# Kernel optimization log

Hardware: AMD Instinct MI355X
Metric: run time of the kernel (lower is better)

Reference implementation:

```python
import jax, jax.numpy as jnp
import numpy as np

B, N, M, C = 2, 8192, 8192, 3
SRC_W = 1.0  # src_weight * loss_src_weight
DST_W = 1.0  # dst_weight * loss_dst_weight


def setup_inputs() -> dict:
    key = jax.random.key(0)
    k1, k2 = jax.random.split(key)
    source = jax.random.normal(k1, (B, N, C), dtype=jnp.float32)
    target = jax.random.normal(k2, (B, M, C), dtype=jnp.float32)
    return {"source": source, "target": target}


def reference(source, target):
    # mode='l2' -> mse_loss(none) summed over C = squared euclidean distance
    # distance: [B, N, M]
    diff = source[:, :, None, :] - target[:, None, :, :]  # [B,N,M,C]
    distance = jnp.sum(diff * diff, axis=-1)
    src2dst = jnp.min(distance, axis=2)       # [B,N]
    indices1 = jnp.argmin(distance, axis=2)   # [B,N]
    dst2src = jnp.min(distance, axis=1)       # [B,M]
    indices2 = jnp.argmin(distance, axis=1)   # [B,M]
    # reduction='mean', weights all 1.0
    loss_src = jnp.mean(src2dst * SRC_W)
    loss_dst = jnp.mean(dst2src * DST_W)
    return (loss_src, loss_dst, indices1, indices2)
```

## Files before the change

kernel.cpp:

```cpp
#include <hip/hip_runtime.h>
#include <math.h>


static constexpr int Bn = 2;
static constexpr int Nn = 8192;
static constexpr int THR = 256;
static constexpr int QPL = 4;
static constexpr int RT = 1024;
static constexpr int WROWS = 256;
static constexpr int CT = 64;
static constexpr int TB = 8;
static constexpr int CB = 4096;

template <int PAT>
__device__ __forceinline__ float swzx(float x) {
    return __int_as_float(__builtin_amdgcn_ds_swizzle(__float_as_int(x), PAT));
}
static constexpr int SWZ_X1  = 0x041F;
static constexpr int SWZ_X2  = 0x081F;
static constexpr int SWZ_X4  = 0x101F;
static constexpr int SWZ_X8  = 0x201F;
static constexpr int SWZ_X16 = 0x401F;

__device__ __forceinline__ float dist3(float s0, float s1, float s2,
                                       float q0, float q1, float q2) {
    #pragma clang fp contract(off)
    float d0 = s0 - q0;
    float d1 = s1 - q1;
    float d2 = s2 - q2;
    return (d0 * d0 + d1 * d1) + d2 * d2;
}

__global__ void cd_init(unsigned long long* __restrict__ ws) {
    int i = blockIdx.x * blockDim.x + threadIdx.x;
    if (i < 2 * Bn * Nn) ws[i] = 0xFFFFFFFFFFFFFFFFULL;
}

__global__ __launch_bounds__(THR) void cd_tile(const float* __restrict__ S,
                                               const float* __restrict__ T,
                                               unsigned long long* __restrict__ ws) {
    const int b = blockIdx.z;
    const int rbase = blockIdx.x * RT;
    const int cbase = blockIdx.y * CT;
    unsigned long long* wsRow = ws + (size_t)b * Nn;
    unsigned long long* wsCol = ws + 2 * Nn + (size_t)b * Nn;

    __shared__ alignas(16) float lq[CT * 3];
    __shared__ unsigned long long lwcol[4][CT];
    if (threadIdx.x < CT * 3 / 4)
        ((float4*)lq)[threadIdx.x] =
            ((const float4*)(T + ((size_t)b * Nn + cbase) * 3))[threadIdx.x];
    __syncthreads();

    const int w = threadIdx.x >> 6;
    const int L = threadIdx.x & 63;
    const int rowA = rbase + w * WROWS + L;
    const unsigned int anchor = (unsigned int)(rbase + w * WROWS);

    float q0[QPL], q1[QPL], q2[QPL];
    #pragma unroll
    for (int k = 0; k < QPL; ++k) {
        const float* p = S + ((size_t)b * Nn + rowA + k * 64) * 3;
        q0[k] = p[0]; q1[k] = p[1]; q2[k] = p[2];
    }

    float best[QPL];
    int bb[QPL];
    #pragma unroll
    for (int k = 0; k < QPL; ++k) { best[k] = INFINITY; bb[k] = 0; }

    const float4* lq4 = (const float4*)lq;
    #pragma unroll 2
    for (int jb = 0; jb < CT / TB; ++jb) {
        float4 v[6];
        #pragma unroll
        for (int j = 0; j < 6; ++j) v[j] = lq4[jb * 6 + j];

        float cm[TB];
        #define COMP(k) ((k & 3) == 0 ? v[(k) >> 2].x : \
                         (k & 3) == 1 ? v[(k) >> 2].y : \
                         (k & 3) == 2 ? v[(k) >> 2].z : v[(k) >> 2].w)
        #pragma unroll
        for (int k = 0; k < QPL; ++k) {
            float d[TB];
            #pragma unroll
            for (int t = 0; t < TB; ++t)
                d[t] = dist3(q0[k], q1[k], q2[k],
                             COMP(3 * t), COMP(3 * t + 1), COMP(3 * t + 2));
            #pragma unroll
            for (int t = 0; t < TB; ++t)
                cm[t] = (k == 0) ? d[t] : fminf(cm[t], d[t]);
            float m0 = fminf(fminf(d[0], d[1]), d[2]);
            float m1 = fminf(fminf(d[3], d[4]), d[5]);
            float m2 = fminf(d[6], d[7]);
            float bmin = fminf(fminf(m0, m1), m2);
            if (bmin < best[k]) { best[k] = bmin; bb[k] = cbase + jb * TB; }
        }
        #undef COMP

        const bool u1 = (L & 1);
        float a0 = fminf(u1 ? cm[4] : cm[0], swzx<SWZ_X1>(u1 ? cm[0] : cm[4]));
        float a1 = fminf(u1 ? cm[5] : cm[1], swzx<SWZ_X1>(u1 ? cm[1] : cm[5]));
        float a2 = fminf(u1 ? cm[6] : cm[2], swzx<SWZ_X1>(u1 ? cm[2] : cm[6]));
        float a3 = fminf(u1 ? cm[7] : cm[3], swzx<SWZ_X1>(u1 ? cm[3] : cm[7]));
        const bool u2 = (L & 2);
        float b0 = fminf(u2 ? a2 : a0, swzx<SWZ_X2>(u2 ? a0 : a2));
        float b1 = fminf(u2 ? a3 : a1, swzx<SWZ_X2>(u2 ? a1 : a3));
        const bool u4 = (L & 4);
        float c0 = fminf(u4 ? b1 : b0, swzx<SWZ_X4>(u4 ? b0 : b1));
        c0 = fminf(c0, swzx<SWZ_X8>(c0));
        c0 = fminf(c0, swzx<SWZ_X16>(c0));
        c0 = fminf(c0, __shfl_xor(c0, 32, 64));

        if (L < TB) {
            const int c = 4 * (L & 1) + 2 * ((L >> 1) & 1) + ((L >> 2) & 1);
            unsigned long long pk =
                ((unsigned long long)__float_as_uint(c0) << 32) | anchor;
            lwcol[w][jb * TB + c] = pk;
        }
    }

    #pragma unroll
    for (int k = 0; k < QPL; ++k) {
        unsigned long long pk =
            ((unsigned long long)__float_as_uint(best[k]) << 32) |
            (unsigned int)bb[k];
        atomicMin(&wsRow[rowA + k * 64], pk);
    }

    __syncthreads();
    if (threadIdx.x < CT) {
        unsigned long long x0 = lwcol[0][threadIdx.x];
        unsigned long long x1 = lwcol[1][threadIdx.x];
        unsigned long long x2 = lwcol[2][threadIdx.x];
        unsigned long long x3 = lwcol[3][threadIdx.x];
        unsigned long long m01 = x0 < x1 ? x0 : x1;
        unsigned long long m23 = x2 < x3 ? x2 : x3;
        unsigned long long m = m01 < m23 ? m01 : m23;
        atomicMin(&wsCol[cbase + threadIdx.x], m);
    }
}

__global__ __launch_bounds__(256) void cd_fin(const unsigned long long* __restrict__ ws,
                                              const float* __restrict__ S,
                                              const float* __restrict__ T,
                                              float* __restrict__ out,
                                              float* __restrict__ pr,
                                              float* __restrict__ pc) {
    __shared__ float red[4];
    const int tid = threadIdx.x;

    if (blockIdx.x < CB) {
        const int e = blockIdx.x * 4 + (tid >> 6);
        const int L = tid & 63;
        const int b = e >> 13;
        const int col = e & 8191;

        unsigned long long p = ws[2 * Nn + e];
        const float m = __uint_as_float((unsigned int)(p >> 32));
        const int A = (int)(unsigned int)(p & 0xFFFFFFFFu);

        const float* tc = T + ((size_t)b * Nn + col) * 3;
        const float t0 = tc[0], t1 = tc[1], t2 = tc[2];

        const float4* Sp = (const float4*)(S + ((size_t)b * Nn + A + L * 4) * 3);
        const float4 x0 = Sp[0], x1 = Sp[1], x2 = Sp[2];

        int found = 0x7FFFFFFF;
        if (dist3(x2.y, x2.z, x2.w, t0, t1, t2) == m) found = A + L * 4 + 3;
        if (dist3(x1.z, x1.w, x2.x, t0, t1, t2) == m) found = A + L * 4 + 2;
        if (dist3(x0.w, x1.x, x1.y, t0, t1, t2) == m) found = A + L * 4 + 1;
        if (dist3(x0.x, x0.y, x0.z, t0, t1, t2) == m) found = A + L * 4 + 0;
        #pragma unroll
        for (int mask = 1; mask < 64; mask <<= 1)
            found = min(found, __shfl_xor(found, mask, 64));
        if (L == 0) out[2 + 2 * Nn + e] = (float)found;

        if (L == 0) red[tid >> 6] = m;
        __syncthreads();
        if (tid == 0) pc[blockIdx.x] = (red[0] + red[1]) + (red[2] + red[3]);
    } else {
        const int j = (blockIdx.x - CB) * 256 + tid;
        const int b = j >> 13;
        const int row = j & 8191;

        unsigned long long p = ws[j];
        const float dist = __uint_as_float((unsigned int)(p >> 32));
        const int cb = (int)(unsigned int)(p & 0xFFFFFFFFu);

        const float* Pp = S + ((size_t)b * Nn + row) * 3;
        const float s0 = Pp[0], s1 = Pp[1], s2 = Pp[2];
        const float4* Qb = (const float4*)(T + ((size_t)b * Nn + cb) * 3);
        const float4 y0 = Qb[0], y1 = Qb[1], y2 = Qb[2];
        const float4 y3 = Qb[3], y4 = Qb[4], y5 = Qb[5];

        int idx = cb;
        if (dist3(s0, s1, s2, y5.y, y5.z, y5.w) == dist) idx = cb + 7;
        if (dist3(s0, s1, s2, y4.z, y4.w, y5.x) == dist) idx = cb + 6;
        if (dist3(s0, s1, s2, y3.w, y4.x, y4.y) == dist) idx = cb + 5;
        if (dist3(s0, s1, s2, y3.x, y3.y, y3.z) == dist) idx = cb + 4;
        if (dist3(s0, s1, s2, y2.y, y2.z, y2.w) == dist) idx = cb + 3;
        if (dist3(s0, s1, s2, y1.z, y1.w, y2.x) == dist) idx = cb + 2;
        if (dist3(s0, s1, s2, y0.w, y1.x, y1.y) == dist) idx = cb + 1;
        if (dist3(s0, s1, s2, y0.x, y0.y, y0.z) == dist) idx = cb + 0;
        out[2 + j] = (float)idx;

        float sum = dist;
        for (int off = 32; off > 0; off >>= 1) sum += __shfl_down(sum, off, 64);
        if ((tid & 63) == 0) red[tid >> 6] = sum;
        __syncthreads();
        if (tid == 0)
            pr[blockIdx.x - CB] = (red[0] + red[1]) + (red[2] + red[3]);
    }
}

__global__ __launch_bounds__(256) void cd_combine(const float* __restrict__ pr,
                                                  const float* __restrict__ pc,
                                                  float* __restrict__ out) {
    const int tid = threadIdx.x;
    float s1 = (tid < 64) ? pr[tid] : 0.0f;
    float s2 = 0.0f;
    for (int i = tid; i < CB; i += 256) s2 += pc[i];

    __shared__ float r1[4], r2[4];
    for (int off = 32; off > 0; off >>= 1) {
        s1 += __shfl_down(s1, off, 64);
        s2 += __shfl_down(s2, off, 64);
    }
    if ((tid & 63) == 0) { r1[tid >> 6] = s1; r2[tid >> 6] = s2; }
    __syncthreads();
    if (tid == 0) {
        out[0] = ((r1[0] + r1[1]) + (r1[2] + r1[3])) / (float)(Bn * Nn);
        out[1] = ((r2[0] + r2[1]) + (r2[2] + r2[3])) / (float)(Bn * Nn);
    }
}

static constexpr int FPTS = 256;
static constexpr int FCHUNK = 1024;

__global__ void cd_zero2(float* __restrict__ out) { out[0] = 0.0f; out[1] = 0.0f; }

__global__ __launch_bounds__(FPTS) void cd_dir_direct(const float* __restrict__ P,
                                                      const float* __restrict__ Q,
                                                      int nP, int nQ,
                                                      float* __restrict__ idx_out,
                                                      float* __restrict__ loss_out,
                                                      float inv_count) {
    __shared__ float lq[FCHUNK * 3];
    __shared__ float red[FPTS / 64];
    const int b = blockIdx.z;
    const int i = blockIdx.x * FPTS + threadIdx.x;
    const float* Pp = P + ((size_t)b * nP + i) * 3;
    const float s0 = Pp[0], s1 = Pp[1], s2 = Pp[2];

    float best = INFINITY;
    int bi = 0;
    for (int c = 0; c < nQ / FCHUNK; ++c) {
        __syncthreads();
        const float* Qb = Q + ((size_t)b * nQ + (size_t)c * FCHUNK) * 3;
        for (int j = threadIdx.x; j < FCHUNK * 3; j += FPTS) lq[j] = Qb[j];
        __syncthreads();
        #pragma unroll 4
        for (int m = 0; m < FCHUNK; ++m) {
            float dist = dist3(s0, s1, s2, lq[3 * m], lq[3 * m + 1], lq[3 * m + 2]);
            if (dist < best) { best = dist; bi = c * FCHUNK + m; }
        }
    }
    idx_out[(size_t)b * nP + i] = (float)bi;

    float v = best;
    for (int off = 32; off > 0; off >>= 1) v += __shfl_down(v, off, 64);
    const int wid = threadIdx.x >> 6;
    if ((threadIdx.x & 63) == 0) red[wid] = v;
    __syncthreads();
    if (threadIdx.x == 0) {
        float a = 0.0f;
        for (int w = 0; w < FPTS / 64; ++w) a += red[w];
        atomicAdd(loss_out, a * inv_count);
    }
}

extern "C" void kernel_launch(void* const* d_in, const int* in_sizes, int n_in,
                              void* d_out, int out_size, void* d_ws, size_t ws_size,
                              hipStream_t stream) {
    const float* src = (const float*)d_in[0];
    const float* tgt = (const float*)d_in[1];
    float* out = (float*)d_out;
    const int TOTAL = 2 * Bn * Nn;
    const size_t need = (size_t)TOTAL * sizeof(unsigned long long)
                      + (64 + CB) * sizeof(float);

    if (ws_size >= need) {
        unsigned long long* ws = (unsigned long long*)d_ws;
        float* pr = (float*)(ws + TOTAL);
        float* pc = pr + 64;
        cd_init<<<(TOTAL + 255) / 256, 256, 0, stream>>>(ws);
        cd_tile<<<dim3(Nn / RT, Nn / CT, Bn), THR, 0, stream>>>(src, tgt, ws);
        cd_fin<<<CB + 64, 256, 0, stream>>>(ws, src, tgt, out, pr, pc);
        cd_combine<<<1, 256, 0, stream>>>(pr, pc, out);
    } else {
        cd_zero2<<<1, 1, 0, stream>>>(out);
        cd_dir_direct<<<dim3(Nn / FPTS, 1, Bn), FPTS, 0, stream>>>(
            src, tgt, Nn, Nn, out + 2, out + 0, 1.0f / (float)(Bn * Nn));
        cd_dir_direct<<<dim3(Nn / FPTS, 1, Bn), FPTS, 0, stream>>>(
            tgt, src, Nn, Nn, out + 2 + Bn * Nn, out + 1, 1.0f / (float)(Bn * Nn));
    }
}
```

Measured before the change: 52.38 us.

## Use packed FP32 math with SoA shared target layout in Chamfer tile kernel

Stores the target tile in shared memory as structure-of-arrays (x, y, z planes) so pairs of target points can be loaded as float2 vectors. Distances are then computed two columns at a time with v_pk_add_f32/v_pk_mul_f32 inline asm, using negated query coordinates so subtraction becomes packed addition. Launch bounds now also request 4 blocks per CU. Packed math should roughly halve the VALU instruction count for the distance computation. The risks are extra register pressure from duplicated query values, and the inline asm limiting compiler scheduling.

```diff
diff --git a/kernel.cpp b/kernel.cpp
--- a/kernel.cpp
+++ b/kernel.cpp
@@ -12,6 +12,35 @@
 static constexpr int TB = 8;
 static constexpr int CB = 4096;
 
+typedef __attribute__((ext_vector_type(2))) float f32x2;
+
+__device__ __forceinline__ f32x2 pk_add(f32x2 a, f32x2 b) {
+    f32x2 r;
+    asm("v_pk_add_f32 %0, %1, %2" : "=v"(r) : "v"(a), "v"(b));
+    return r;
+}
+__device__ __forceinline__ f32x2 pk_mul(f32x2 a, f32x2 b) {
+    f32x2 r;
+    asm("v_pk_mul_f32 %0, %1, %2" : "=v"(r) : "v"(a), "v"(b));
+    return r;
+}
+__device__ __forceinline__ f32x2 fmin2(f32x2 a, f32x2 b) {
+    f32x2 r;
+    r.x = fminf(a.x, b.x);
+    r.y = fminf(a.y, b.y);
+    return r;
+}
+__device__ __forceinline__ f32x2 dist3x2(f32x2 tx, f32x2 ty, f32x2 tz,
+                                         f32x2 nqx, f32x2 nqy, f32x2 nqz) {
+    f32x2 dx = pk_add(tx, nqx);
+    f32x2 dy = pk_add(ty, nqy);
+    f32x2 dz = pk_add(tz, nqz);
+    f32x2 px = pk_mul(dx, dx);
+    f32x2 py = pk_mul(dy, dy);
+    f32x2 pz = pk_mul(dz, dz);
+    return pk_add(pk_add(px, py), pz);
+}
+
 template <int PAT>
 __device__ __forceinline__ float swzx(float x) {
     return __int_as_float(__builtin_amdgcn_ds_swizzle(__float_as_int(x), PAT));
@@ -36,20 +65,25 @@
     if (i < 2 * Bn * Nn) ws[i] = 0xFFFFFFFFFFFFFFFFULL;
 }
 
-__global__ __launch_bounds__(THR) void cd_tile(const float* __restrict__ S,
-                                               const float* __restrict__ T,
-                                               unsigned long long* __restrict__ ws) {
+__global__ __launch_bounds__(THR, 4) void cd_tile(const float* __restrict__ S,
+                                                  const float* __restrict__ T,
+                                                  unsigned long long* __restrict__ ws) {
     const int b = blockIdx.z;
     const int rbase = blockIdx.x * RT;
     const int cbase = blockIdx.y * CT;
     unsigned long long* wsRow = ws + (size_t)b * Nn;
     unsigned long long* wsCol = ws + 2 * Nn + (size_t)b * Nn;
 
-    __shared__ alignas(16) float lq[CT * 3];
+    __shared__ alignas(16) float lt[3][CT];
     __shared__ unsigned long long lwcol[4][CT];
-    if (threadIdx.x < CT * 3 / 4)
-        ((float4*)lq)[threadIdx.x] =
-            ((const float4*)(T + ((size_t)b * Nn + cbase) * 3))[threadIdx.x];
+    if (threadIdx.x < CT * 3 / 4) {
+        float4 v4 = ((const float4*)(T + ((size_t)b * Nn + cbase) * 3))[threadIdx.x];
+        int e = threadIdx.x * 4;
+        lt[(e    ) % 3][(e    ) / 3] = v4.x;
+        lt[(e + 1) % 3][(e + 1) / 3] = v4.y;
+        lt[(e + 2) % 3][(e + 2) / 3] = v4.z;
+        lt[(e + 3) % 3][(e + 3) / 3] = v4.w;
+    }
     __syncthreads();
 
     const int w = threadIdx.x >> 6;
@@ -57,11 +91,14 @@
     const int rowA = rbase + w * WROWS + L;
     const unsigned int anchor = (unsigned int)(rbase + w * WROWS);
 
-    float q0[QPL], q1[QPL], q2[QPL];
+    f32x2 nqx[QPL], nqy[QPL], nqz[QPL];
     #pragma unroll
     for (int k = 0; k < QPL; ++k) {
         const float* p = S + ((size_t)b * Nn + rowA + k * 64) * 3;
-        q0[k] = p[0]; q1[k] = p[1]; q2[k] = p[2];
+        float a0 = -p[0], a1 = -p[1], a2 = -p[2];
+        nqx[k].x = a0; nqx[k].y = a0;
+        nqy[k].x = a1; nqy[k].y = a1;
+        nqz[k].x = a2; nqz[k].y = a2;
     }
 
     float best[QPL];
@@ -69,40 +106,40 @@
     #pragma unroll
     for (int k = 0; k < QPL; ++k) { best[k] = INFINITY; bb[k] = 0; }
 
-    const float4* lq4 = (const float4*)lq;
     #pragma unroll 2
     for (int jb = 0; jb < CT / TB; ++jb) {
-        float4 v[6];
+        const f32x2* lx = (const f32x2*)&lt[0][jb * TB];
+        const f32x2* ly = (const f32x2*)&lt[1][jb * TB];
+        const f32x2* lz = (const f32x2*)&lt[2][jb * TB];
+        f32x2 tx[4], ty[4], tz[4];
         #pragma unroll
-        for (int j = 0; j < 6; ++j) v[j] = lq4[jb * 6 + j];
-
-        float cm[TB];
-        #define COMP(k) ((k & 3) == 0 ? v[(k) >> 2].x : \
-                         (k & 3) == 1 ? v[(k) >> 2].y : \
-                         (k & 3) == 2 ? v[(k) >> 2].z : v[(k) >> 2].w)
+        for (int p = 0; p < 4; ++p) { tx[p] = lx[p]; ty[p] = ly[p]; tz[p] = lz[p]; }
+
+        f32x2 cm2[4];
         #pragma unroll
         for (int k = 0; k < QPL; ++k) {
-            float d[TB];
+            f32x2 dd[4];
             #pragma unroll
-            for (int t = 0; t < TB; ++t)
-                d[t] = dist3(q0[k], q1[k], q2[k],
-                             COMP(3 * t), COMP(3 * t + 1), COMP(3 * t + 2));
+            for (int p = 0; p < 4; ++p)
+                dd[p] = dist3x2(tx[p], ty[p], tz[p], nqx[k], nqy[k], nqz[k]);
             #pragma unroll
-            for (int t = 0; t < TB; ++t)
-                cm[t] = (k == 0) ? d[t] : fminf(cm[t], d[t]);
-            float m0 = fminf(fminf(d[0], d[1]), d[2]);
-            float m1 = fminf(fminf(d[3], d[4]), d[5]);
-            float m2 = fminf(d[6], d[7]);
+            for (int p = 0; p < 4; ++p)
+                cm2[p] = (k == 0) ? dd[p] : fmin2(cm2[p], dd[p]);
+            float m0 = fminf(fminf(dd[0].x, dd[0].y), dd[1].x);
+            float m1 = fminf(fminf(dd[1].y, dd[2].x), dd[2].y);
+            float m2 = fminf(dd[3].x, dd[3].y);
             float bmin = fminf(fminf(m0, m1), m2);
             if (bmin < best[k]) { best[k] = bmin; bb[k] = cbase + jb * TB; }
         }
-        #undef COMP
+
+        float cmf0 = cm2[0].x, cmf1 = cm2[0].y, cmf2 = cm2[1].x, cmf3 = cm2[1].y;
+        float cmf4 = cm2[2].x, cmf5 = cm2[2].y, cmf6 = cm2[3].x, cmf7 = cm2[3].y;
 
         const bool u1 = (L & 1);
-        float a0 = fminf(u1 ? cm[4] : cm[0], swzx<SWZ_X1>(u1 ? cm[0] : cm[4]));
-        float a1 = fminf(u1 ? cm[5] : cm[1], swzx<SWZ_X1>(u1 ? cm[1] : cm[5]));
-        float a2 = fminf(u1 ? cm[6] : cm[2], swzx<SWZ_X1>(u1 ? cm[2] : cm[6]));
-        float a3 = fminf(u1 ? cm[7] : cm[3], swzx<SWZ_X1>(u1 ? cm[3] : cm[7]));
+        float a0 = fminf(u1 ? cmf4 : cmf0, swzx<SWZ_X1>(u1 ? cmf0 : cmf4));
+        float a1 = fminf(u1 ? cmf5 : cmf1, swzx<SWZ_X1>(u1 ? cmf1 : cmf5));
+        float a2 = fminf(u1 ? cmf6 : cmf2, swzx<SWZ_X1>(u1 ? cmf2 : cmf6));
+        float a3 = fminf(u1 ? cmf7 : cmf3, swzx<SWZ_X1>(u1 ? cmf3 : cmf7));
         const bool u2 = (L & 2);
         float b0 = fminf(u2 ? a2 : a0, swzx<SWZ_X2>(u2 ? a0 : a2));
         float b1 = fminf(u2 ? a3 : a1, swzx<SWZ_X2>(u2 ? a1 : a3));
```

Result: slower. 54.59 us (+4.2%).
